# Kernel tuning notes

Measured on AMD Instinct MI355X. Metric: run time of the kernel, lower is better.

The kernel has to match this reference:

```python
import jax, jax.numpy as jnp
import numpy as np

NUM_FEAT = 64        # per-head dim == input channel C
HIDDEN = 1024        # total hidden size
NUM_HEADS = HIDDEN // NUM_FEAT  # 16


def setup_inputs() -> dict:
    key = jax.random.key(0)
    k1, k2, k3, k4, k5 = jax.random.split(key, 5)
    B, N, C = 4, 2048, NUM_FEAT
    hidden_states = jax.random.normal(k1, (B, N, C), dtype=jnp.float32)
    # nn.Linear(num_feat, hidden*3): weight [3*hidden, num_feat], store transposed for x @ W
    s_qkv = 1.0 / np.sqrt(C)
    qkv_w = jax.random.uniform(k2, (C, 3 * HIDDEN), jnp.float32, -s_qkv, s_qkv)
    qkv_b = jax.random.uniform(k3, (3 * HIDDEN,), jnp.float32, -s_qkv, s_qkv)
    s_out = 1.0 / np.sqrt(HIDDEN)
    out_w = jax.random.uniform(k4, (HIDDEN, C), jnp.float32, -s_out, s_out)
    out_b = jax.random.uniform(k5, (C,), jnp.float32, -s_out, s_out)
    return {"hidden_states": hidden_states, "qkv_w": qkv_w, "qkv_b": qkv_b,
            "out_w": out_w, "out_b": out_b}


def reference(hidden_states, qkv_w, qkv_b, out_w, out_b):
    B, N, C = hidden_states.shape
    H, D = NUM_HEADS, NUM_FEAT  # head count, head dim
    # qkv projection: [B,N,3*HIDDEN] -> [3,B,H,N,D]
    qkv = hidden_states @ qkv_w + qkv_b
    qkv = qkv.reshape(B, N, 3, H, D).transpose(2, 0, 3, 1, 4)
    q, k, v = qkv[0], qkv[1], qkv[2]
    # scaled dot-product attention with materialized scores (faithful to source)
    scores = jnp.einsum('bhqd,bhkd->bhqk', q, k) / jnp.sqrt(jnp.float32(D))
    probs = jax.nn.softmax(scores, axis=-1)
    ctx = jnp.einsum('bhqk,bhkd->bhqd', probs, v)           # [B,H,N,D]
    ctx = ctx.transpose(0, 2, 1, 3).reshape(B, N, H * D)    # [B,N,HIDDEN]
    out = ctx @ out_w + out_b                               # [B,N,C]
    return jax.nn.gelu(out, approximate=False)
```

## Files before the change

kernel.cpp:

```cpp
#include <hip/hip_runtime.h>
#include <math.h>

#define B_ 4
#define N_ 2048
#define C_ 64
#define H_ 16
#define D_ 64
#define HID 1024

#define QSCALE 0.18033688011112042f

typedef short bf16x8 __attribute__((ext_vector_type(8)));
typedef unsigned short u16x8 __attribute__((ext_vector_type(8)));
typedef float f32x4 __attribute__((ext_vector_type(4)));
typedef unsigned u32x4 __attribute__((ext_vector_type(4)));

#define MFMA(a, b, c) __builtin_amdgcn_mfma_f32_16x16x32_bf16((a), (b), (c), 0, 0, 0)

typedef __attribute__((address_space(3))) void lds_t;
typedef const __attribute__((address_space(1))) void gbl_t;
#define ASYNC16(g, l) __builtin_amdgcn_global_load_lds((gbl_t*)(g), (lds_t*)(l), 16, 0, 0)

static __device__ __forceinline__ unsigned short f2bf(float f) {
  unsigned u = __float_as_uint(f);
  u += 0x7FFFu + ((u >> 16) & 1u);
  return (unsigned short)(u >> 16);
}
static __device__ __forceinline__ float bf2f(unsigned short h) {
  return __uint_as_float((unsigned)h << 16);
}
static __device__ __forceinline__ unsigned pkbf(float a, float b) {
  return __builtin_amdgcn_perm(__float_as_uint(b), __float_as_uint(a),
                               0x07060302u);
}

__global__ __launch_bounds__(256, 2) void qkv_kernel(
    const float* __restrict__ X, const float* __restrict__ W,
    const float* __restrict__ bias, const float* __restrict__ W2,
    unsigned short* __restrict__ Qhi, unsigned short* __restrict__ Khi,
    unsigned short* __restrict__ Vhi,
    unsigned short* __restrict__ W2THi, unsigned short* __restrict__ W2TLo) {
  const int t = threadIdx.x;
  const int ct = blockIdx.x;
  const int tt = blockIdx.y;

  if (ct == 24) {
    int idx0 = tt * 1024 + t * 4;
#pragma unroll
    for (int e = 0; e < 4; ++e) {
      int idx = idx0 + e;
      int k = idx & 1023, col = idx >> 10;
      float v = W2[(size_t)k * 64 + col];
      unsigned short hi = f2bf(v);
      W2THi[(size_t)col * 1024 + k] = hi;
      W2TLo[(size_t)col * 1024 + k] = f2bf(v - bf2f(hi));
    }
    return;
  }

  __shared__ unsigned short qsmem[32768];
  unsigned short* sXhi = qsmem;
  unsigned short* sXlo = qsmem + 8192;
  unsigned short* sWhi = qsmem + 16384;
  unsigned short* sWlo = qsmem + 24576;

  {
    const int kg = t & 7, r0 = t >> 3;
#pragma unroll
    for (int i = 0; i < 4; ++i) {
      int row = r0 + i * 32;
      const float* src = &X[(size_t)(tt * 128 + row) * 64 + kg * 8];
      f32x4 a = *(const f32x4*)src;
      f32x4 b = *(const f32x4*)(src + 4);
      u16x8 hi8, lo8;
#pragma unroll
      for (int j = 0; j < 4; ++j) {
        hi8[j] = f2bf(a[j]);
        lo8[j] = f2bf(a[j] - bf2f(hi8[j]));
        hi8[4 + j] = f2bf(b[j]);
        lo8[4 + j] = f2bf(b[j] - bf2f(hi8[4 + j]));
      }
      int off = row * 64 + ((kg ^ (row & 7)) << 3);
      *(u16x8*)&sXhi[off] = hi8;
      *(u16x8*)&sXlo[off] = lo8;
    }
  }
  {
    const int col = t & 127, kg0 = t >> 7;
#pragma unroll
    for (int i = 0; i < 4; ++i) {
      int kg = kg0 + i * 2;
      u16x8 hi8, lo8;
#pragma unroll
      for (int j = 0; j < 8; ++j) {
        float v = W[(size_t)(kg * 8 + j) * 3072 + ct * 128 + col];
        unsigned short h = f2bf(v);
        hi8[j] = h;
        lo8[j] = f2bf(v - bf2f(h));
      }
      int off = col * 64 + ((kg ^ (col & 7)) << 3);
      *(u16x8*)&sWhi[off] = hi8;
      *(u16x8*)&sWlo[off] = lo8;
    }
  }
  __syncthreads();

  const int w = t >> 6, lane = t & 63;
  const int lid = lane & 15, quad = lane >> 4;

  bf16x8 xa[2][2][2];
#pragma unroll
  for (int mt = 0; mt < 2; ++mt) {
    int row = w * 32 + mt * 16 + lid;
#pragma unroll
    for (int kc = 0; kc < 2; ++kc) {
      int off = row * 64 + (((kc * 4 + quad) ^ (row & 7)) << 3);
      xa[mt][kc][0] = *(const bf16x8*)&sXhi[off];
      xa[mt][kc][1] = *(const bf16x8*)&sXlo[off];
    }
  }

  f32x4 acc[2][8];
#pragma unroll
  for (int mt = 0; mt < 2; ++mt)
#pragma unroll
    for (int nt = 0; nt < 8; ++nt) acc[mt][nt] = (f32x4){0.f, 0.f, 0.f, 0.f};

#pragma unroll
  for (int nt = 0; nt < 8; ++nt) {
    int col = nt * 16 + lid;
#pragma unroll
    for (int kc = 0; kc < 2; ++kc) {
      int boff = col * 64 + (((kc * 4 + quad) ^ (col & 7)) << 3);
      bf16x8 wbh = *(const bf16x8*)&sWhi[boff];
      bf16x8 wbl = *(const bf16x8*)&sWlo[boff];
#pragma unroll
      for (int mt = 0; mt < 2; ++mt) {
        f32x4 c = acc[mt][nt];
        c = MFMA(xa[mt][kc][0], wbh, c);
        c = MFMA(xa[mt][kc][0], wbl, c);
        c = MFMA(xa[mt][kc][1], wbh, c);
        acc[mt][nt] = c;
      }
    }
  }

  __syncthreads();

  const int s = ct >> 3;
  const float scale = (s == 0) ? QSCALE : 1.0f;
  float bias_r[8];
#pragma unroll
  for (int nt = 0; nt < 8; ++nt) bias_r[nt] = bias[ct * 128 + nt * 16 + lid];

  if (s < 2) {
    unsigned short(*sOut)[136] = (unsigned short(*)[136])qsmem;
#pragma unroll
    for (int mt = 0; mt < 2; ++mt)
#pragma unroll
      for (int nt = 0; nt < 8; ++nt) {
        f32x4 v = acc[mt][nt];
#pragma unroll
        for (int r = 0; r < 4; ++r)
          sOut[w * 32 + mt * 16 + quad * 4 + r][nt * 16 + lid] =
              f2bf((v[r] + bias_r[nt]) * scale);
      }
    __syncthreads();
    const int ltok = t >> 1, half = t & 1;
    const int token = tt * 128 + ltok;
    const int bb = token >> 11, n = token & 2047;
    const int head = (ct * 2 + half) & 15;
    unsigned short* A = (s == 0) ? Qhi : Khi;
    size_t dst = ((size_t)(bb * H_ + head) * N_ + n) * D_;
    const unsigned short* srcr = &sOut[ltok][half * 64];
#pragma unroll
    for (int j = 0; j < 8; ++j)
      *(uint4*)&A[dst + j * 8] = *(const uint4*)&srcr[j * 8];
  } else {
    unsigned short(*sT)[136] = (unsigned short(*)[136])qsmem;
#pragma unroll
    for (int mt = 0; mt < 2; ++mt)
#pragma unroll
      for (int nt = 0; nt < 8; ++nt) {
        f32x4 v = acc[mt][nt];
        unsigned short h0 = f2bf(v[0] + bias_r[nt]);
        unsigned short h1 = f2bf(v[1] + bias_r[nt]);
        unsigned short h2 = f2bf(v[2] + bias_r[nt]);
        unsigned short h3 = f2bf(v[3] + bias_r[nt]);
        uint2 dw;
        dw.x = (unsigned)h0 | ((unsigned)h1 << 16);
        dw.y = (unsigned)h2 | ((unsigned)h3 << 16);
        int a = mt * 4 + quad;
        int ap = ((a & 3) * 2) + (a >> 2);
        *(uint2*)&sT[nt * 16 + lid][w * 32 + ap * 4] = dw;
      }
    __syncthreads();
    const int col = t >> 1, half = t & 1;
    const int hv = (ct & 7) * 2 + (col >> 6), d = col & 63;
    const int bbv = tt >> 4;
    const int n0 = (tt & 15) * 128 + half * 64;
    size_t row = (size_t)((bbv * H_ + hv) * D_ + d);
    unsigned short* dstp = Vhi + row * (size_t)N_ + n0;
    const unsigned short* srcr = &sT[col][half * 64];
#pragma unroll
    for (int j = 0; j < 8; ++j)
      *(uint4*)(dstp + j * 8) = *(const uint4*)&srcr[j * 8];
  }
}

__global__ __launch_bounds__(256, 4) void attn_kernel(
    const unsigned short* __restrict__ Qhi, const unsigned short* __restrict__ Khi,
    const unsigned short* __restrict__ VThi,
    unsigned short* __restrict__ ctxHi, unsigned short* __restrict__ ctxLo) {
  __shared__ unsigned short smem[12288];

  const int tid = threadIdx.x;
  const int w = tid >> 6, lane = tid & 63;
  const int lid = lane & 15, quad = lane >> 4;
  const int l7 = lid & 7;
  unsigned short* sK = smem;
  unsigned short* sVt = smem + 6144;

  const int id = blockIdx.x;
  const int bh = id & 63;
  const int qt = id >> 6;
  const int b = bh >> 4, h = bh & 15;
  const size_t base = (size_t)bh * N_ * D_;
  const int row0 = qt * 128 + w * 32;

  bf16x8 qh[2][2];
#pragma unroll
  for (int mt = 0; mt < 2; ++mt) {
    int row = row0 + mt * 16 + lid;
    const unsigned short* qph = Qhi + base + (size_t)row * D_;
#pragma unroll
    for (int kc = 0; kc < 2; ++kc)
      qh[mt][kc] = *(const bf16x8*)(qph + kc * 32 + quad * 8);
  }

  f32x4 o[2][4];
  float lacc[2] = {0.f, 0.f};
#pragma unroll
  for (int mt = 0; mt < 2; ++mt)
#pragma unroll
    for (int dnt = 0; dnt < 4; ++dnt) o[mt][dnt] = (f32x4){0.f, 0.f, 0.f, 0.f};

  const int lrow = lane >> 3;
  const int lgr = (lane & 7) ^ lrow;

  auto stage = [&](int kt_, int buf_) {
    size_t gk = base + (size_t)(kt_ * 32 + w * 8 + lrow) * 64 + lgr * 8;
    ASYNC16(Khi + gk, sK + buf_ * 2048 + (w * 8) * 64);
    int pr = w * 8 + lrow;
    int vd = pr * 2 + (lgr >> 2);
    int vk0 = (lgr & 3) * 8;
    size_t gv = base + (size_t)vd * N_ + kt_ * 32 + vk0;
    ASYNC16(VThi + gv, sVt + buf_ * 2048 + (w * 8) * 64);
  };

  const int NT = N_ / 32;
  stage(0, 0);
  stage(1, 1);

  int cur = 0;
  for (int kt = 0; kt < NT; ++kt) {
    if (kt < NT - 1)
      asm volatile("s_waitcnt vmcnt(2)" ::: "memory");
    else
      asm volatile("s_waitcnt vmcnt(0)" ::: "memory");
    __builtin_amdgcn_s_barrier();
    __builtin_amdgcn_sched_barrier(0);
    if (kt + 2 < NT) {
      int nxt2 = cur >= 1 ? cur - 1 : cur + 2;
      stage(kt + 2, nxt2);
    }
    const int buf = cur;

    f32x4 sc[2][2];
    __builtin_amdgcn_s_setprio(1);
#pragma unroll
    for (int nt = 0; nt < 2; ++nt) {
      int key = nt * 16 + lid;
#pragma unroll
      for (int kc = 0; kc < 2; ++kc) {
        int off = key * 64 + (((kc * 4 + quad) ^ l7) << 3);
        bf16x8 kh_ = *(const bf16x8*)&sK[buf * 2048 + off];
#pragma unroll
        for (int mt = 0; mt < 2; ++mt) {
          f32x4 c = (kc == 0) ? (f32x4){0.f, 0.f, 0.f, 0.f} : sc[mt][nt];
          c = MFMA(kh_, qh[mt][kc], c);
          sc[mt][nt] = c;
        }
      }
    }
    __builtin_amdgcn_s_setprio(0);

    bf16x8 pa[2];
#pragma unroll
    for (int mt = 0; mt < 2; ++mt) {
      float lsum = 0.f;
      u32x4 pw;
#pragma unroll
      for (int nt = 0; nt < 2; ++nt) {
        float p0 = __builtin_amdgcn_exp2f(sc[mt][nt][0]);
        float p1 = __builtin_amdgcn_exp2f(sc[mt][nt][1]);
        float p2 = __builtin_amdgcn_exp2f(sc[mt][nt][2]);
        float p3 = __builtin_amdgcn_exp2f(sc[mt][nt][3]);
        lsum += (p0 + p1) + (p2 + p3);
        pw[nt * 2 + 0] = pkbf(p0, p1);
        pw[nt * 2 + 1] = pkbf(p2, p3);
      }
      lacc[mt] += lsum;
      pa[mt] = __builtin_bit_cast(bf16x8, pw);
    }

    __builtin_amdgcn_s_setprio(1);
#pragma unroll
    for (int dnt = 0; dnt < 4; ++dnt) {
      int voff = buf * 2048 + (dnt * 8 + (lid >> 1)) * 64 +
                 (((quad + (lid & 1) * 4) ^ ((lid >> 1) & 7)) << 3);
      bf16x8 vh = *(const bf16x8*)&sVt[voff];
#pragma unroll
      for (int mt = 0; mt < 2; ++mt) o[mt][dnt] = MFMA(vh, pa[mt], o[mt][dnt]);
    }
    __builtin_amdgcn_s_setprio(0);

    cur = cur == 2 ? 0 : cur + 1;
  }

#pragma unroll
  for (int mt = 0; mt < 2; ++mt) {
    lacc[mt] += __shfl_xor(lacc[mt], 16);
    lacc[mt] += __shfl_xor(lacc[mt], 32);
  }

  __syncthreads();
  float* scr = (float*)smem + w * 1088;
  const int erow = lane >> 2, ecq = lane & 3;
#pragma unroll
  for (int mt = 0; mt < 2; ++mt) {
    float inv = 1.0f / lacc[mt];
#pragma unroll
    for (int dnt = 0; dnt < 4; ++dnt) {
      f32x4 v = o[mt][dnt] * inv;
      *(f32x4*)&scr[lid * 68 + dnt * 16 + quad * 4] = v;
    }
    int token = b * N_ + row0 + mt * 16 + erow;
    size_t doff = (size_t)token * HID + h * 64;
#pragma unroll
    for (int i = 0; i < 4; ++i) {
      f32x4 v4 = *(const f32x4*)&scr[erow * 68 + ecq * 4 + i * 16];
      unsigned short hi_[4], lo_[4];
#pragma unroll
      for (int j = 0; j < 4; ++j) {
        hi_[j] = f2bf(v4[j]);
        lo_[j] = f2bf(v4[j] - bf2f(hi_[j]));
      }
      uint2 hw, lw;
      hw.x = (unsigned)hi_[0] | ((unsigned)hi_[1] << 16);
      hw.y = (unsigned)hi_[2] | ((unsigned)hi_[3] << 16);
      lw.x = (unsigned)lo_[0] | ((unsigned)lo_[1] << 16);
      lw.y = (unsigned)lo_[2] | ((unsigned)lo_[3] << 16);
      *(uint2*)&ctxHi[doff + ecq * 4 + i * 16] = hw;
      *(uint2*)&ctxLo[doff + ecq * 4 + i * 16] = lw;
    }
  }
}

__global__ __launch_bounds__(256) void out_kernel(
    const unsigned short* __restrict__ ctxHi, const unsigned short* __restrict__ ctxLo,
    const unsigned short* __restrict__ W2THi, const unsigned short* __restrict__ W2TLo,
    const float* __restrict__ b2, float* __restrict__ out) {
  __shared__ float sO[4][4][16][16];
  const int tid = threadIdx.x;
  const int w = tid >> 6, lane = tid & 63;
  const int lid = lane & 15, quad = lane >> 4;
  const int tok0 = blockIdx.x * 16;

  f32x4 acc[4];
#pragma unroll
  for (int nt = 0; nt < 4; ++nt) acc[nt] = (f32x4){0.f, 0.f, 0.f, 0.f};

  const size_t abase = (size_t)(tok0 + lid) * HID + w * 256 + quad * 8;

  for (int kc = 0; kc < 8; ++kc) {
    bf16x8 ah = *(const bf16x8*)&ctxHi[abase + kc * 32];
    bf16x8 al = *(const bf16x8*)&ctxLo[abase + kc * 32];
#pragma unroll
    for (int nt = 0; nt < 4; ++nt) {
      size_t boff =
          (size_t)(nt * 16 + lid) * HID + w * 256 + kc * 32 + quad * 8;
      bf16x8 bh = *(const bf16x8*)&W2THi[boff];
      bf16x8 bl = *(const bf16x8*)&W2TLo[boff];
      f32x4 c = acc[nt];
      c = MFMA(ah, bh, c);
      c = MFMA(ah, bl, c);
      c = MFMA(al, bh, c);
      acc[nt] = c;
    }
  }

#pragma unroll
  for (int nt = 0; nt < 4; ++nt)
#pragma unroll
    for (int r = 0; r < 4; ++r) sO[w][nt][quad * 4 + r][lid] = acc[nt][r];
  __syncthreads();

  const int col = tid & 63;
  const int nt = col >> 4, cl = col & 15;
#pragma unroll
  for (int rr = 0; rr < 4; ++rr) {
    int row = w * 4 + rr;
    float v = sO[0][nt][row][cl] + sO[1][nt][row][cl] + sO[2][nt][row][cl] +
              sO[3][nt][row][cl] + b2[col];
    float g = 0.5f * v * (1.0f + erff(v * 0.70710678118654752f));
    out[(size_t)(tok0 + row) * 64 + col] = g;
  }
}

extern "C" void kernel_launch(void* const* d_in, const int* in_sizes, int n_in,
                              void* d_out, int out_size, void* d_ws, size_t ws_size,
                              hipStream_t stream) {
  const float* X = (const float*)d_in[0];
  const float* qkv_w = (const float*)d_in[1];
  const float* qkv_b = (const float*)d_in[2];
  const float* out_w = (const float*)d_in[3];
  const float* out_b = (const float*)d_in[4];
  float* out = (float*)d_out;

  const size_t NE = (size_t)B_ * H_ * N_ * D_;
  unsigned short* ws16 = (unsigned short*)d_ws;
  unsigned short* Qhi = ws16 + 0 * NE;
  unsigned short* Khi = ws16 + 1 * NE;
  unsigned short* VThi = ws16 + 2 * NE;
  unsigned short* ctxHi = ws16 + 3 * NE;
  unsigned short* ctxLo = ws16 + 4 * NE;
  unsigned short* W2THi = ws16 + 5 * NE;
  unsigned short* W2TLo = W2THi + 65536;

  qkv_kernel<<<dim3(25, 64), 256, 0, stream>>>(X, qkv_w, qkv_b, out_w, Qhi,
                                               Khi, VThi, W2THi, W2TLo);
  attn_kernel<<<1024, 256, 0, stream>>>(Qhi, Khi, VThi, ctxHi, ctxLo);
  out_kernel<<<512, 256, 0, stream>>>(ctxHi, ctxLo, W2THi, W2TLo, out_b, out);
}
```

Before: 192.7 us.

## Double the attention key tile to 64 and switch to double buffering

Each loop iteration now processes 64 keys instead of 32, halving the number of barrier and wait iterations. The K/V staging moves from a three-slot ring with partial vmcnt waits to two buffers with a full vmcnt(0) wait, and the V^T LDS layout and swizzle are simplified. The aim is to amortise synchronisation and increase MFMA work per barrier. In exchange, LDS grows to 32KB per block, the score registers double, and the full wait leaves less load latency hidden, which may cost occupancy at four blocks per CU.

```diff
diff --git a/kernel.cpp b/kernel.cpp
--- a/kernel.cpp
+++ b/kernel.cpp
@@ -212,14 +212,14 @@
     const unsigned short* __restrict__ Qhi, const unsigned short* __restrict__ Khi,
     const unsigned short* __restrict__ VThi,
     unsigned short* __restrict__ ctxHi, unsigned short* __restrict__ ctxLo) {
-  __shared__ unsigned short smem[12288];
+  __shared__ unsigned short smem[16384];
 
   const int tid = threadIdx.x;
   const int w = tid >> 6, lane = tid & 63;
   const int lid = lane & 15, quad = lane >> 4;
   const int l7 = lid & 7;
   unsigned short* sK = smem;
-  unsigned short* sVt = smem + 6144;
+  unsigned short* sVt = smem + 8192;
 
   const int id = blockIdx.x;
   const int bh = id & 63;
@@ -249,83 +249,85 @@
   const int lgr = (lane & 7) ^ lrow;
 
   auto stage = [&](int kt_, int buf_) {
-    size_t gk = base + (size_t)(kt_ * 32 + w * 8 + lrow) * 64 + lgr * 8;
-    ASYNC16(Khi + gk, sK + buf_ * 2048 + (w * 8) * 64);
-    int pr = w * 8 + lrow;
-    int vd = pr * 2 + (lgr >> 2);
-    int vk0 = (lgr & 3) * 8;
-    size_t gv = base + (size_t)vd * N_ + kt_ * 32 + vk0;
-    ASYNC16(VThi + gv, sVt + buf_ * 2048 + (w * 8) * 64);
+#pragma unroll
+    for (int i = 0; i < 2; ++i) {
+      size_t gk =
+          base + (size_t)(kt_ * 64 + w * 16 + i * 8 + lrow) * 64 + lgr * 8;
+      ASYNC16(Khi + gk, sK + buf_ * 4096 + (w * 16 + i * 8) * 64);
+    }
+#pragma unroll
+    for (int i = 0; i < 2; ++i) {
+      int d = w * 16 + i * 8 + lrow;
+      size_t gv = base + (size_t)d * N_ + kt_ * 64 + lgr * 8;
+      ASYNC16(VThi + gv, sVt + buf_ * 4096 + (w * 16 + i * 8) * 64);
+    }
   };
 
-  const int NT = N_ / 32;
+  const int NT = N_ / 64;
   stage(0, 0);
-  stage(1, 1);
-
-  int cur = 0;
+
   for (int kt = 0; kt < NT; ++kt) {
-    if (kt < NT - 1)
-      asm volatile("s_waitcnt vmcnt(2)" ::: "memory");
-    else
-      asm volatile("s_waitcnt vmcnt(0)" ::: "memory");
+    const int buf = kt & 1;
+    asm volatile("s_waitcnt vmcnt(0)" ::: "memory");
     __builtin_amdgcn_s_barrier();
     __builtin_amdgcn_sched_barrier(0);
-    if (kt + 2 < NT) {
-      int nxt2 = cur >= 1 ? cur - 1 : cur + 2;
-      stage(kt + 2, nxt2);
-    }
-    const int buf = cur;
-
-    f32x4 sc[2][2];
+    if (kt + 1 < NT) stage(kt + 1, buf ^ 1);
+
+    f32x4 sc[2][4];
     __builtin_amdgcn_s_setprio(1);
 #pragma unroll
-    for (int nt = 0; nt < 2; ++nt) {
+    for (int nt = 0; nt < 4; ++nt) {
       int key = nt * 16 + lid;
 #pragma unroll
       for (int kc = 0; kc < 2; ++kc) {
-        int off = key * 64 + (((kc * 4 + quad) ^ l7) << 3);
-        bf16x8 kh_ = *(const bf16x8*)&sK[buf * 2048 + off];
+        int off = buf * 4096 + key * 64 + (((kc * 4 + quad) ^ l7) << 3);
+        bf16x8 kh_ = *(const bf16x8*)&sK[off];
 #pragma unroll
         for (int mt = 0; mt < 2; ++mt) {
           f32x4 c = (kc == 0) ? (f32x4){0.f, 0.f, 0.f, 0.f} : sc[mt][nt];
-          c = MFMA(kh_, qh[mt][kc], c);
-          sc[mt][nt] = c;
+          sc[mt][nt] = MFMA(kh_, qh[mt][kc], c);
         }
       }
     }
     __builtin_amdgcn_s_setprio(0);
 
-    bf16x8 pa[2];
+    bf16x8 pa[2][2];
 #pragma unroll
     for (int mt = 0; mt < 2; ++mt) {
       float lsum = 0.f;
-      u32x4 pw;
-#pragma unroll
-      for (int nt = 0; nt < 2; ++nt) {
-        float p0 = __builtin_amdgcn_exp2f(sc[mt][nt][0]);
-        float p1 = __builtin_amdgcn_exp2f(sc[mt][nt][1]);
-        float p2 = __builtin_amdgcn_exp2f(sc[mt][nt][2]);
-        float p3 = __builtin_amdgcn_exp2f(sc[mt][nt][3]);
-        lsum += (p0 + p1) + (p2 + p3);
-        pw[nt * 2 + 0] = pkbf(p0, p1);
-        pw[nt * 2 + 1] = pkbf(p2, p3);
+#pragma unroll
+      for (int hf = 0; hf < 2; ++hf) {
+        u32x4 pw;
+#pragma unroll
+        for (int nth = 0; nth < 2; ++nth) {
+          int nt = hf * 2 + nth;
+          float p0 = __builtin_amdgcn_exp2f(sc[mt][nt][0]);
+          float p1 = __builtin_amdgcn_exp2f(sc[mt][nt][1]);
+          float p2 = __builtin_amdgcn_exp2f(sc[mt][nt][2]);
+          float p3 = __builtin_amdgcn_exp2f(sc[mt][nt][3]);
+          lsum += (p0 + p1) + (p2 + p3);
+          pw[nth * 2 + 0] = pkbf(p0, p1);
+          pw[nth * 2 + 1] = pkbf(p2, p3);
+        }
+        pa[mt][hf] = __builtin_bit_cast(bf16x8, pw);
       }
       lacc[mt] += lsum;
-      pa[mt] = __builtin_bit_cast(bf16x8, pw);
     }
 
     __builtin_amdgcn_s_setprio(1);
 #pragma unroll
     for (int dnt = 0; dnt < 4; ++dnt) {
-      int voff = buf * 2048 + (dnt * 8 + (lid >> 1)) * 64 +
-                 (((quad + (lid & 1) * 4) ^ ((lid >> 1) & 7)) << 3);
-      bf16x8 vh = *(const bf16x8*)&sVt[voff];
-#pragma unroll
-      for (int mt = 0; mt < 2; ++mt) o[mt][dnt] = MFMA(vh, pa[mt], o[mt][dnt]);
+#pragma unroll
+      for (int hf = 0; hf < 2; ++hf) {
+        int voff = buf * 4096 + (dnt * 16 + lid) * 64 +
+                   (((hf * 4 + quad) ^ l7) << 3);
+        bf16x8 vh = *(const bf16x8*)&sVt[voff];
+#pragma unroll
+        for (int mt = 0; mt < 2; ++mt)
+          o[mt][dnt] = MFMA(vh, pa[mt][hf], o[mt][dnt]);
+      }
     }
     __builtin_amdgcn_s_setprio(0);
-
-    cur = cur == 2 ? 0 : cur + 1;
   }
 
 #pragma unroll
```

Result: no change. 193.1 us (+0.2%).

## Software-pipeline attention loop: overlap next tile's QK with current PV, 4-deep buffering

Applied to the files above, without the earlier changes.

Restructures the attention inner loop so that the QK^T score MFMAs for tile k+1 are issued together with the PV MFMAs for tile k. The exp/pack softmax step then runs after them, interleaved with the next pair. The loop is unrolled by two with ping-pong probability registers. The K/V LDS ring grows from 3 to 4 buffers so three tiles can be in flight. The intent is to hide exp latency and the dependency between S and PV behind matrix work. The cost is more LDS per block, which could reduce occupancy, and higher register pressure.

```diff
diff --git a/kernel.cpp b/kernel.cpp
--- a/kernel.cpp
+++ b/kernel.cpp
@@ -212,14 +212,14 @@
     const unsigned short* __restrict__ Qhi, const unsigned short* __restrict__ Khi,
     const unsigned short* __restrict__ VThi,
     unsigned short* __restrict__ ctxHi, unsigned short* __restrict__ ctxLo) {
-  __shared__ unsigned short smem[12288];
+  __shared__ unsigned short smem[16384];
 
   const int tid = threadIdx.x;
   const int w = tid >> 6, lane = tid & 63;
   const int lid = lane & 15, quad = lane >> 4;
   const int l7 = lid & 7;
   unsigned short* sK = smem;
-  unsigned short* sVt = smem + 6144;
+  unsigned short* sVt = smem + 8192;
 
   const int id = blockIdx.x;
   const int bh = id & 63;
@@ -258,44 +258,24 @@
     ASYNC16(VThi + gv, sVt + buf_ * 2048 + (w * 8) * 64);
   };
 
-  const int NT = N_ / 32;
-  stage(0, 0);
-  stage(1, 1);
-
-  int cur = 0;
-  for (int kt = 0; kt < NT; ++kt) {
-    if (kt < NT - 1)
-      asm volatile("s_waitcnt vmcnt(2)" ::: "memory");
-    else
-      asm volatile("s_waitcnt vmcnt(0)" ::: "memory");
-    __builtin_amdgcn_s_barrier();
-    __builtin_amdgcn_sched_barrier(0);
-    if (kt + 2 < NT) {
-      int nxt2 = cur >= 1 ? cur - 1 : cur + 2;
-      stage(kt + 2, nxt2);
-    }
-    const int buf = cur;
-
-    f32x4 sc[2][2];
-    __builtin_amdgcn_s_setprio(1);
+  auto doS = [&](int buf, f32x4 (&sc)[2][2]) {
 #pragma unroll
     for (int nt = 0; nt < 2; ++nt) {
       int key = nt * 16 + lid;
 #pragma unroll
       for (int kc = 0; kc < 2; ++kc) {
-        int off = key * 64 + (((kc * 4 + quad) ^ l7) << 3);
-        bf16x8 kh_ = *(const bf16x8*)&sK[buf * 2048 + off];
+        int off = buf * 2048 + key * 64 + (((kc * 4 + quad) ^ l7) << 3);
+        bf16x8 kh_ = *(const bf16x8*)&sK[off];
 #pragma unroll
         for (int mt = 0; mt < 2; ++mt) {
           f32x4 c = (kc == 0) ? (f32x4){0.f, 0.f, 0.f, 0.f} : sc[mt][nt];
-          c = MFMA(kh_, qh[mt][kc], c);
-          sc[mt][nt] = c;
+          sc[mt][nt] = MFMA(kh_, qh[mt][kc], c);
         }
       }
     }
-    __builtin_amdgcn_s_setprio(0);
-
-    bf16x8 pa[2];
+  };
+
+  auto doP = [&](f32x4 (&sc)[2][2], bf16x8 (&pa)[2]) {
 #pragma unroll
     for (int mt = 0; mt < 2; ++mt) {
       float lsum = 0.f;
@@ -313,8 +293,9 @@
       lacc[mt] += lsum;
       pa[mt] = __builtin_bit_cast(bf16x8, pw);
     }
-
-    __builtin_amdgcn_s_setprio(1);
+  };
+
+  auto doPV = [&](int buf, bf16x8 (&pa)[2]) {
 #pragma unroll
     for (int dnt = 0; dnt < 4; ++dnt) {
       int voff = buf * 2048 + (dnt * 8 + (lid >> 1)) * 64 +
@@ -323,9 +304,47 @@
 #pragma unroll
       for (int mt = 0; mt < 2; ++mt) o[mt][dnt] = MFMA(vh, pa[mt], o[mt][dnt]);
     }
+  };
+
+  const int NT = N_ / 32;
+  stage(0, 0);
+  stage(1, 1);
+  stage(2, 2);
+  asm volatile("s_waitcnt vmcnt(4)" ::: "memory");
+  __builtin_amdgcn_s_barrier();
+  __builtin_amdgcn_sched_barrier(0);
+
+  f32x4 sc[2][2];
+  bf16x8 paA[2], paB[2];
+  doS(0, sc);
+  doP(sc, paA);
+
+  for (int kt = 0; kt < NT; kt += 2) {
+    if (kt + 2 < NT)
+      asm volatile("s_waitcnt vmcnt(2)" ::: "memory");
+    else
+      asm volatile("s_waitcnt vmcnt(0)" ::: "memory");
+    __builtin_amdgcn_s_barrier();
+    __builtin_amdgcn_sched_barrier(0);
+    if (kt + 3 < NT) stage(kt + 3, (kt + 3) & 3);
+    __builtin_amdgcn_s_setprio(1);
+    doS((kt + 1) & 3, sc);
+    doPV(kt & 3, paA);
     __builtin_amdgcn_s_setprio(0);
-
-    cur = cur == 2 ? 0 : cur + 1;
+    doP(sc, paB);
+
+    if (kt + 3 < NT)
+      asm volatile("s_waitcnt vmcnt(2)" ::: "memory");
+    else
+      asm volatile("s_waitcnt vmcnt(0)" ::: "memory");
+    __builtin_amdgcn_s_barrier();
+    __builtin_amdgcn_sched_barrier(0);
+    if (kt + 4 < NT) stage(kt + 4, (kt + 4) & 3);
+    __builtin_amdgcn_s_setprio(1);
+    if (kt + 2 < NT) doS((kt + 2) & 3, sc);
+    doPV((kt + 1) & 3, paB);
+    __builtin_amdgcn_s_setprio(0);
+    if (kt + 2 < NT) doP(sc, paA);
   }
 
 #pragma unroll
```

After: 192.3 us. Within noise of the previous version (-0.2%).
